# Optimization experiments

Hardware: AMD Instinct MI355X
Metric: run time of the kernel (lower is better)

## Reference

```python
import jax, jax.numpy as jnp
import numpy as np

W_CLS, W_BBOX, W_GIOU = 1.0, 5.0, 2.0
EPS = 1e-06


def _cxcywh_to_xyxy(box):
    cx, cy, w, h = box[..., 0], box[..., 1], box[..., 2], box[..., 3]
    return jnp.stack([cx - 0.5 * w, cy - 0.5 * h, cx + 0.5 * w, cy + 0.5 * h], axis=-1)


def _giou(b1, b2):
    # b1: [B, N, 4] xyxy, b2: [B, M, 4] xyxy -> giou [B, N, M]
    area1 = jnp.clip(b1[..., 2] - b1[..., 0], 0) * jnp.clip(b1[..., 3] - b1[..., 1], 0)  # [B,N]
    area2 = jnp.clip(b2[..., 2] - b2[..., 0], 0) * jnp.clip(b2[..., 3] - b2[..., 1], 0)  # [B,M]
    lt = jnp.maximum(b1[:, :, None, :2], b2[:, None, :, :2])  # [B,N,M,2]
    rb = jnp.minimum(b1[:, :, None, 2:], b2[:, None, :, 2:])
    wh = jnp.clip(rb - lt, 0)
    inter = wh[..., 0] * wh[..., 1]
    union = area1[:, :, None] + area2[:, None, :] - inter + EPS
    iou = inter / union
    lt_enc = jnp.minimum(b1[:, :, None, :2], b2[:, None, :, :2])
    rb_enc = jnp.maximum(b1[:, :, None, 2:], b2[:, None, :, 2:])
    wh_enc = jnp.clip(rb_enc - lt_enc, 0)
    enc = wh_enc[..., 0] * wh_enc[..., 1] + EPS
    return iou - (enc - union) / enc


def setup_inputs() -> dict:
    key = jax.random.key(0)
    k1, k2, k3, k4 = jax.random.split(key, 4)
    B, NQ, C, NT = 64, 900, 256, 128
    return {
        "pred_logits": jax.random.normal(k1, (B, NQ, C), dtype=jnp.float32),
        "pred_boxes": jax.random.uniform(k2, (B, NQ, 4), dtype=jnp.float32),
        "tgt_labels": jax.random.randint(k3, (B, NT), 0, C),
        "tgt_boxes": jax.random.uniform(k4, (B, NT, 4), dtype=jnp.float32),
    }


def reference(pred_logits, pred_boxes, tgt_labels, tgt_boxes):
    B, NQ, _ = pred_logits.shape
    NT = tgt_labels.shape[1]
    out_prob = jax.nn.softmax(pred_logits, axis=-1)  # [B,NQ,C]
    # gather class probs at target label ids: [B,NQ,NT]
    idx = jnp.broadcast_to(tgt_labels[:, None, :], (B, NQ, NT))
    cost_cls = -jnp.take_along_axis(out_prob, idx, axis=-1)
    # L1 cdist over cxcywh coords: [B,NQ,NT]
    cost_bbox = jnp.sum(jnp.abs(pred_boxes[:, :, None, :] - tgt_boxes[:, None, :, :]), axis=-1)
    giou = _giou(_cxcywh_to_xyxy(pred_boxes), _cxcywh_to_xyxy(tgt_boxes))
    cost_giou = -giou
    C = W_CLS * cost_cls + W_BBOX * cost_bbox + W_GIOU * cost_giou
    return C
```

## Files before the change

kernel.cpp:

```cpp
#include <hip/hip_runtime.h>

#define BB   64
#define NQ   900
#define NC   256
#define NT   128

#define RPW  4
#define RPB  16
#define NCHUNK 57

typedef float f32x2 __attribute__((ext_vector_type(2)));

template<int CTRL>
__device__ __forceinline__ float dpp_add(float x) {
    int y = __builtin_amdgcn_update_dpp(0, __float_as_int(x), CTRL, 0xF, 0xF, true);
    return x + __int_as_float(y);
}

__device__ __forceinline__ float lane_bcast(float x, int l) {
    return __int_as_float(__builtin_amdgcn_readlane(__float_as_int(x), l));
}

__global__ __launch_bounds__(256, 4) void matcher_kernel(
    const float* __restrict__ logits,
    const float* __restrict__ pboxes,
    const int*   __restrict__ tlabels,
    const float* __restrict__ tboxes,
    float* __restrict__ out)
{
    constexpr float W_BBOX = 5.0f, W_GIOU = 2.0f, EPS = 1e-6f;

    __shared__ __align__(16) float raw[RPB][NC];

    const int wave = threadIdx.x >> 6;
    const int lane = threadIdx.x & 63;
    const int g    = lane >> 4;
    const int j    = lane & 15;
    const int b    = blockIdx.y;
    const int q0   = blockIdx.x * RPB + wave * RPW;
    if (q0 >= NQ) return;
    const int wr0  = wave * RPW;

    int qg = q0 + g; qg = qg < NQ - 1 ? qg : NQ - 1;
    const float* lrow = logits + ((size_t)b * NQ + qg) * NC + j * 4;
    const float4 v0 = *reinterpret_cast<const float4*>(lrow);
    const float4 v1 = *reinterpret_cast<const float4*>(lrow + 64);
    const float4 v2 = *reinterpret_cast<const float4*>(lrow + 128);
    const float4 v3 = *reinterpret_cast<const float4*>(lrow + 192);

    float4 pb[RPW];
    #pragma unroll
    for (int r = 0; r < RPW; ++r)
        pb[r] = *reinterpret_cast<const float4*>(pboxes + ((size_t)b * NQ + q0 + r) * 4);

    const int t0 = lane * 2;
    const int2   lbl = *reinterpret_cast<const int2*>(tlabels + b * NT + t0);
    const float4 ta  = *reinterpret_cast<const float4*>(tboxes + ((size_t)b * NT + t0) * 4);
    const float4 tbv = *reinterpret_cast<const float4*>(tboxes + ((size_t)b * NT + t0 + 1) * 4);

    float* srow = &raw[wr0 + g][j * 4];
    *reinterpret_cast<float4*>(srow)       = v0;
    *reinterpret_cast<float4*>(srow + 64)  = v1;
    *reinterpret_cast<float4*>(srow + 128) = v2;
    *reinterpret_cast<float4*>(srow + 192) = v3;

    float ga[RPW], gb[RPW];
    #pragma unroll
    for (int r = 0; r < RPW; ++r) {
        ga[r] = raw[wr0 + r][lbl.x];
        gb[r] = raw[wr0 + r][lbl.y];
    }

    float s = (((__expf(v0.x) + __expf(v0.y)) + (__expf(v0.z) + __expf(v0.w)))
            +  ((__expf(v1.x) + __expf(v1.y)) + (__expf(v1.z) + __expf(v1.w))))
            + (((__expf(v2.x) + __expf(v2.y)) + (__expf(v2.z) + __expf(v2.w)))
            +  ((__expf(v3.x) + __expf(v3.y)) + (__expf(v3.z) + __expf(v3.w))));
    s = dpp_add<0xB1>(s);
    s = dpp_add<0x4E>(s);
    s = dpp_add<0x141>(s);
    s = dpp_add<0x140>(s);

    const float inv[RPW] = {
        __builtin_amdgcn_rcpf(lane_bcast(s, 0)),
        __builtin_amdgcn_rcpf(lane_bcast(s, 16)),
        __builtin_amdgcn_rcpf(lane_bcast(s, 32)),
        __builtin_amdgcn_rcpf(lane_bcast(s, 48)) };

    const float ax1 = ta.x - 0.5f * ta.z, ay1 = ta.y - 0.5f * ta.w;
    const float ax2 = ta.x + 0.5f * ta.z, ay2 = ta.y + 0.5f * ta.w;
    const float aarea = fmaxf(ax2 - ax1, 0.0f) * fmaxf(ay2 - ay1, 0.0f);
    const float bx1 = tbv.x - 0.5f * tbv.z, by1 = tbv.y - 0.5f * tbv.w;
    const float bx2 = tbv.x + 0.5f * tbv.z, by2 = tbv.y + 0.5f * tbv.w;
    const float barea = fmaxf(bx2 - bx1, 0.0f) * fmaxf(by2 - by1, 0.0f);

    #pragma unroll
    for (int r = 0; r < RPW; ++r) {
        const float p0 = __expf(ga[r]) * inv[r];
        const float p1 = __expf(gb[r]) * inv[r];

        const float px1 = pb[r].x - 0.5f * pb[r].z, py1 = pb[r].y - 0.5f * pb[r].w;
        const float px2 = pb[r].x + 0.5f * pb[r].z, py2 = pb[r].y + 0.5f * pb[r].w;
        const float parea = fmaxf(px2 - px1, 0.0f) * fmaxf(py2 - py1, 0.0f);

        const float l1a = fabsf(pb[r].x - ta.x) + fabsf(pb[r].y - ta.y)
                        + fabsf(pb[r].z - ta.z) + fabsf(pb[r].w - ta.w);
        const float ia  = fmaxf(fminf(px2, ax2) - fmaxf(px1, ax1), 0.0f)
                        * fmaxf(fminf(py2, ay2) - fmaxf(py1, ay1), 0.0f);
        const float ua  = parea + aarea - ia + EPS;
        const float ea  = fmaxf(fmaxf(px2, ax2) - fminf(px1, ax1), 0.0f)
                        * fmaxf(fmaxf(py2, ay2) - fminf(py1, ay1), 0.0f) + EPS;
        const float gioua = ia * __builtin_amdgcn_rcpf(ua)
                          - (ea - ua) * __builtin_amdgcn_rcpf(ea);
        const float c0 = -p0 + W_BBOX * l1a - W_GIOU * gioua;

        const float l1b = fabsf(pb[r].x - tbv.x) + fabsf(pb[r].y - tbv.y)
                        + fabsf(pb[r].z - tbv.z) + fabsf(pb[r].w - tbv.w);
        const float ib  = fmaxf(fminf(px2, bx2) - fmaxf(px1, bx1), 0.0f)
                        * fmaxf(fminf(py2, by2) - fmaxf(py1, by1), 0.0f);
        const float ub  = parea + barea - ib + EPS;
        const float eb  = fmaxf(fmaxf(px2, bx2) - fminf(px1, bx1), 0.0f)
                        * fmaxf(fmaxf(py2, by2) - fminf(py1, by1), 0.0f) + EPS;
        const float gioub = ib * __builtin_amdgcn_rcpf(ub)
                          - (eb - ub) * __builtin_amdgcn_rcpf(eb);
        const float c1 = -p1 + W_BBOX * l1b - W_GIOU * gioub;

        f32x2 cc; cc.x = c0; cc.y = c1;
        __builtin_nontemporal_store(cc,
            reinterpret_cast<f32x2*>(out + ((size_t)b * NQ + q0 + r) * NT + t0));
    }
}

extern "C" void kernel_launch(void* const* d_in, const int* in_sizes, int n_in,
                              void* d_out, int out_size, void* d_ws, size_t ws_size,
                              hipStream_t stream) {
    const float* logits  = (const float*)d_in[0];
    const float* pboxes  = (const float*)d_in[1];
    const int*   tlabels = (const int*)d_in[2];
    const float* tboxes  = (const float*)d_in[3];
    float* out = (float*)d_out;

    dim3 grid(NCHUNK, BB);
    matcher_kernel<<<grid, 256, 0, stream>>>(logits, pboxes, tlabels, tboxes, out);
}
```

Baseline: 20.90 us.

## Process two row groups per block with async global-to-LDS prefetch of second

```diff
diff --git a/kernel.cpp b/kernel.cpp
--- a/kernel.cpp
+++ b/kernel.cpp
@@ -7,9 +7,11 @@
 
 #define RPW  4
 #define RPB  16
-#define NCHUNK 57
+#define NBX  29
 
 typedef float f32x2 __attribute__((ext_vector_type(2)));
+typedef const __attribute__((address_space(1))) void gas_t;
+typedef __attribute__((address_space(3))) void las_t;
 
 template<int CTRL>
 __device__ __forceinline__ float dpp_add(float x) {
@@ -30,61 +32,48 @@
 {
     constexpr float W_BBOX = 5.0f, W_GIOU = 2.0f, EPS = 1e-6f;
 
-    __shared__ __align__(16) float raw[RPB][NC];
+    __shared__ __align__(16) float raw [RPB][NC];
+    __shared__ __align__(16) float raw2[RPB][NC];
 
     const int wave = threadIdx.x >> 6;
     const int lane = threadIdx.x & 63;
     const int g    = lane >> 4;
     const int j    = lane & 15;
     const int b    = blockIdx.y;
-    const int q0   = blockIdx.x * RPB + wave * RPW;
-    if (q0 >= NQ) return;
     const int wr0  = wave * RPW;
-
-    int qg = q0 + g; qg = qg < NQ - 1 ? qg : NQ - 1;
-    const float* lrow = logits + ((size_t)b * NQ + qg) * NC + j * 4;
+    const int q0a  = blockIdx.x * (2 * RPB) + wr0;
+    const int q0b  = q0a + RPB;
+
+    const size_t rowbase = (size_t)b * NQ;
+
+    #pragma unroll
+    for (int k = 0; k < RPW; ++k) {
+        int q = q0b + k; q = q < NQ - 1 ? q : NQ - 1;
+        const float* src = logits + (rowbase + q) * NC + lane * 4;
+        __builtin_amdgcn_global_load_lds((gas_t*)src, (las_t*)&raw2[wr0 + k][0],
+                                         16, 0, 0);
+    }
+
+    int qg = q0a + g; qg = qg < NQ - 1 ? qg : NQ - 1;
+    const float* lrow = logits + (rowbase + qg) * NC + j * 4;
     const float4 v0 = *reinterpret_cast<const float4*>(lrow);
     const float4 v1 = *reinterpret_cast<const float4*>(lrow + 64);
     const float4 v2 = *reinterpret_cast<const float4*>(lrow + 128);
     const float4 v3 = *reinterpret_cast<const float4*>(lrow + 192);
 
-    float4 pb[RPW];
+    float4 pba[RPW], pbb[RPW];
     #pragma unroll
-    for (int r = 0; r < RPW; ++r)
-        pb[r] = *reinterpret_cast<const float4*>(pboxes + ((size_t)b * NQ + q0 + r) * 4);
+    for (int r = 0; r < RPW; ++r) {
+        int qa = q0a + r; qa = qa < NQ - 1 ? qa : NQ - 1;
+        int qb = q0b + r; qb = qb < NQ - 1 ? qb : NQ - 1;
+        pba[r] = *reinterpret_cast<const float4*>(pboxes + (rowbase + qa) * 4);
+        pbb[r] = *reinterpret_cast<const float4*>(pboxes + (rowbase + qb) * 4);
+    }
 
     const int t0 = lane * 2;
     const int2   lbl = *reinterpret_cast<const int2*>(tlabels + b * NT + t0);
     const float4 ta  = *reinterpret_cast<const float4*>(tboxes + ((size_t)b * NT + t0) * 4);
     const float4 tbv = *reinterpret_cast<const float4*>(tboxes + ((size_t)b * NT + t0 + 1) * 4);
-
-    float* srow = &raw[wr0 + g][j * 4];
-    *reinterpret_cast<float4*>(srow)       = v0;
-    *reinterpret_cast<float4*>(srow + 64)  = v1;
-    *reinterpret_cast<float4*>(srow + 128) = v2;
-    *reinterpret_cast<float4*>(srow + 192) = v3;
-
-    float ga[RPW], gb[RPW];
-    #pragma unroll
-    for (int r = 0; r < RPW; ++r) {
-        ga[r] = raw[wr0 + r][lbl.x];
-        gb[r] = raw[wr0 + r][lbl.y];
-    }
-
-    float s = (((__expf(v0.x) + __expf(v0.y)) + (__expf(v0.z) + __expf(v0.w)))
-            +  ((__expf(v1.x) + __expf(v1.y)) + (__expf(v1.z) + __expf(v1.w))))
-            + (((__expf(v2.x) + __expf(v2.y)) + (__expf(v2.z) + __expf(v2.w)))
-            +  ((__expf(v3.x) + __expf(v3.y)) + (__expf(v3.z) + __expf(v3.w))));
-    s = dpp_add<0xB1>(s);
-    s = dpp_add<0x4E>(s);
-    s = dpp_add<0x141>(s);
-    s = dpp_add<0x140>(s);
-
-    const float inv[RPW] = {
-        __builtin_amdgcn_rcpf(lane_bcast(s, 0)),
-        __builtin_amdgcn_rcpf(lane_bcast(s, 16)),
-        __builtin_amdgcn_rcpf(lane_bcast(s, 32)),
-        __builtin_amdgcn_rcpf(lane_bcast(s, 48)) };
 
     const float ax1 = ta.x - 0.5f * ta.z, ay1 = ta.y - 0.5f * ta.w;
     const float ax2 = ta.x + 0.5f * ta.z, ay2 = ta.y + 0.5f * ta.w;
@@ -93,17 +82,16 @@
     const float bx2 = tbv.x + 0.5f * tbv.z, by2 = tbv.y + 0.5f * tbv.w;
     const float barea = fmaxf(bx2 - bx1, 0.0f) * fmaxf(by2 - by1, 0.0f);
 
-    #pragma unroll
-    for (int r = 0; r < RPW; ++r) {
-        const float p0 = __expf(ga[r]) * inv[r];
-        const float p1 = __expf(gb[r]) * inv[r];
-
-        const float px1 = pb[r].x - 0.5f * pb[r].z, py1 = pb[r].y - 0.5f * pb[r].w;
-        const float px2 = pb[r].x + 0.5f * pb[r].z, py2 = pb[r].y + 0.5f * pb[r].w;
+    auto cost_store = [&](const float4& pb, float p0e, float p1e, float invs, int q) {
+        const float p0 = p0e * invs;
+        const float p1 = p1e * invs;
+
+        const float px1 = pb.x - 0.5f * pb.z, py1 = pb.y - 0.5f * pb.w;
+        const float px2 = pb.x + 0.5f * pb.z, py2 = pb.y + 0.5f * pb.w;
         const float parea = fmaxf(px2 - px1, 0.0f) * fmaxf(py2 - py1, 0.0f);
 
-        const float l1a = fabsf(pb[r].x - ta.x) + fabsf(pb[r].y - ta.y)
-                        + fabsf(pb[r].z - ta.z) + fabsf(pb[r].w - ta.w);
+        const float l1a = fabsf(pb.x - ta.x) + fabsf(pb.y - ta.y)
+                        + fabsf(pb.z - ta.z) + fabsf(pb.w - ta.w);
         const float ia  = fmaxf(fminf(px2, ax2) - fmaxf(px1, ax1), 0.0f)
                         * fmaxf(fminf(py2, ay2) - fmaxf(py1, ay1), 0.0f);
         const float ua  = parea + aarea - ia + EPS;
@@ -113,8 +101,8 @@
                           - (ea - ua) * __builtin_amdgcn_rcpf(ea);
         const float c0 = -p0 + W_BBOX * l1a - W_GIOU * gioua;
 
-        const float l1b = fabsf(pb[r].x - tbv.x) + fabsf(pb[r].y - tbv.y)
-                        + fabsf(pb[r].z - tbv.z) + fabsf(pb[r].w - tbv.w);
+        const float l1b = fabsf(pb.x - tbv.x) + fabsf(pb.y - tbv.y)
+                        + fabsf(pb.z - tbv.z) + fabsf(pb.w - tbv.w);
         const float ib  = fmaxf(fminf(px2, bx2) - fmaxf(px1, bx1), 0.0f)
                         * fmaxf(fminf(py2, by2) - fmaxf(py1, by1), 0.0f);
         const float ub  = parea + barea - ib + EPS;
@@ -126,7 +114,78 @@
 
         f32x2 cc; cc.x = c0; cc.y = c1;
         __builtin_nontemporal_store(cc,
-            reinterpret_cast<f32x2*>(out + ((size_t)b * NQ + q0 + r) * NT + t0));
+            reinterpret_cast<f32x2*>(out + (rowbase + q) * NT + t0));
+    };
+
+    {
+        float* srow = &raw[wr0 + g][j * 4];
+        *reinterpret_cast<float4*>(srow)       = v0;
+        *reinterpret_cast<float4*>(srow + 64)  = v1;
+        *reinterpret_cast<float4*>(srow + 128) = v2;
+        *reinterpret_cast<float4*>(srow + 192) = v3;
+
+        float ga[RPW], gb[RPW];
+        #pragma unroll
+        for (int r = 0; r < RPW; ++r) {
+            ga[r] = raw[wr0 + r][lbl.x];
+            gb[r] = raw[wr0 + r][lbl.y];
+        }
+
+        float s = (((__expf(v0.x) + __expf(v0.y)) + (__expf(v0.z) + __expf(v0.w)))
+                +  ((__expf(v1.x) + __expf(v1.y)) + (__expf(v1.z) + __expf(v1.w))))
+                + (((__expf(v2.x) + __expf(v2.y)) + (__expf(v2.z) + __expf(v2.w)))
+                +  ((__expf(v3.x) + __expf(v3.y)) + (__expf(v3.z) + __expf(v3.w))));
+        s = dpp_add<0xB1>(s); s = dpp_add<0x4E>(s);
+        s = dpp_add<0x141>(s); s = dpp_add<0x140>(s);
+
+        const float inv[RPW] = {
+            __builtin_amdgcn_rcpf(lane_bcast(s, 0)),
+            __builtin_amdgcn_rcpf(lane_bcast(s, 16)),
+            __builtin_amdgcn_rcpf(lane_bcast(s, 32)),
+            __builtin_amdgcn_rcpf(lane_bcast(s, 48)) };
+
+        if (q0a < NQ) {
+            #pragma unroll
+            for (int r = 0; r < RPW; ++r)
+                cost_store(pba[r], __expf(ga[r]), __expf(gb[r]), inv[r], q0a + r);
+        }
+    }
+
+    asm volatile("s_waitcnt vmcnt(4)" ::: "memory");
+    __builtin_amdgcn_sched_barrier(0);
+
+    {
+        float ga[RPW], gb[RPW];
+        #pragma unroll
+        for (int r = 0; r < RPW; ++r) {
+            ga[r] = raw2[wr0 + r][lbl.x];
+            gb[r] = raw2[wr0 + r][lbl.y];
+        }
+
+        const float* rr = &raw2[wr0 + g][j * 4];
+        const float4 w0 = *reinterpret_cast<const float4*>(rr);
+        const float4 w1 = *reinterpret_cast<const float4*>(rr + 64);
+        const float4 w2 = *reinterpret_cast<const float4*>(rr + 128);
+        const float4 w3 = *reinterpret_cast<const float4*>(rr + 192);
+
+        float s = (((__expf(w0.x) + __expf(w0.y)) + (__expf(w0.z) + __expf(w0.w)))
+                +  ((__expf(w1.x) + __expf(w1.y)) + (__expf(w1.z) + __expf(w1.w))))
+                + (((__expf(w2.x) + __expf(w2.y)) + (__expf(w2.z) + __expf(w2.w)))
+                +  ((__expf(w3.x) + __expf(w3.y)) + (__expf(w3.z) + __expf(w3.w))));
+        s = dpp_add<0xB1>(s); s = dpp_add<0x4E>(s);
+        s = dpp_add<0x141>(s); s = dpp_add<0x140>(s);
+
+        const float inv[RPW] = {
+            __builtin_amdgcn_rcpf(lane_bcast(s, 0)),
+            __builtin_amdgcn_rcpf(lane_bcast(s, 16)),
+            __builtin_amdgcn_rcpf(lane_bcast(s, 32)),
+            __builtin_amdgcn_rcpf(lane_bcast(s, 48)) };
+
+        if (q0b < NQ) {
+            #pragma unroll
+            for (int r = 0; r < RPW; ++r)
+                cost_store(pbb[r], __expf(ga[r]), __expf(gb[r]), inv[r], q0b + r);
+        }
     }
 }
 
@@ -139,6 +198,6 @@
     const float* tboxes  = (const float*)d_in[3];
     float* out = (float*)d_out;
 
-    dim3 grid(NCHUNK, BB);
+    dim3 grid(NBX, BB);
     matcher_kernel<<<grid, 256, 0, stream>>>(logits, pboxes, tlabels, tboxes, out);
 }
```

Result: slower. 22.40 us (+7.2%).
